# Kernel optimization log

Hardware: AMD Instinct MI355X
Metric: run time of the kernel (lower is better)

Reference implementation:

```python
import jax, jax.numpy as jnp
from jax import lax
import numpy as np

ALPHA = 0.5
MAX_ITERS = 40
TOL = 1e-6
BITS = 8


def fake_quant_sym(w, bits=BITS):
    # symmetric per-tensor fake quantisation
    qmax = float(2 ** (bits - 1) - 1)
    scale = jnp.max(jnp.abs(w)) / qmax
    return jnp.round(w / scale) * scale


def fb_solve(Wq, Uq, bq, x, alpha=ALPHA, max_iters=MAX_ITERS, tol=TOL):
    # forward-backward splitting fixed-point solve: z = relu((1-a)z + a(Wz + Ux^T + b))
    n = Wq.shape[0]
    B = x.shape[0]
    Ux = Uq @ x.T + bq[:, None]  # (n, B), constant across iterations

    def cond(carry):
        z, res, it = carry
        return jnp.logical_and(it < max_iters, res >= tol)

    def body(carry):
        z, _, it = carry
        u = (1.0 - alpha) * z + alpha * (Wq @ z + Ux)
        z_next = jax.nn.relu(u)  # relu_prox
        res = jnp.linalg.norm(z_next - z) / (jnp.linalg.norm(z) + 1e-12)
        return z_next, res, it + 1

    z0 = jnp.zeros((n, B), dtype=x.dtype)
    z, _, _ = lax.while_loop(cond, body, (z0, jnp.array(jnp.inf, dtype=x.dtype), 0))
    u_star = (1.0 - alpha) * z + alpha * (Wq @ z + Ux)
    mask = (u_star > 0).astype(x.dtype)  # relu Jacobian mask D*
    return z, mask


def setup_inputs() -> dict:
    key = jax.random.key(0)
    k0, k1, k2, k3, k4 = jax.random.split(key, 5)
    n, d, B, C = 512, 784, 128, 10
    # scale W so ||W||_2 < 1 (monotone operator condition m > 0)
    W = 0.3 * jax.random.normal(k0, (n, n), dtype=jnp.float32) / jnp.sqrt(n)
    U = jax.random.normal(k1, (n, d), dtype=jnp.float32) / jnp.sqrt(d)
    b = 0.01 * jax.random.normal(k2, (n,), dtype=jnp.float32)
    x = jax.random.normal(k3, (B, d), dtype=jnp.float32)
    Wc = jax.random.normal(k4, (C, n), dtype=jnp.float32) / jnp.sqrt(n)
    bc = jnp.zeros((C,), dtype=jnp.float32)
    return {"W": W, "U": U, "b": b, "x": x, "Wc": Wc, "bc": bc}


def reference(W, U, b, x, Wc, bc):
    # post-training fake quantisation of W, U, b (done once at init in torch)
    Wq = fake_quant_sym(W)
    Uq = fake_quant_sym(U)
    bq = fake_quant_sym(b)
    z_star, _ = fb_solve(Wq, Uq, bq, x)  # (n, B)
    logits = z_star.T @ Wc.T + bc  # classifier on z*^T
    return logits
```

## Files before the change

kernel.cpp:

```cpp
#include <hip/hip_runtime.h>
#include <hip/hip_bf16.h>


#define N_DIM 512
#define D_DIM 784
#define B_DIM 128
#define C_DIM 10
#define QMAX 127.0f
#define N_ITERS 40
#define HILO_START 28
#define ZPITCH 528
#define MT 2
#define XPITCH 800
#define QUPITCH 808

typedef int    i32x4  __attribute__((ext_vector_type(4)));
typedef float  f32x4  __attribute__((ext_vector_type(4)));
typedef __bf16 bf16x8 __attribute__((ext_vector_type(8)));
typedef short  s16x2  __attribute__((ext_vector_type(2)));

#define WSF_PW  0
#define WSF_PU  64
#define WSF_SB  128
#define WSF_CNT 160
#define WSF_BQ  192
#define WSF_XH  704
#define WSF_XL  (WSF_XH + 51200)
#define WSF_QP8 (WSF_XL + 51200)
#define WSF_UXT (WSF_QP8 + 65536)

#define N_PRODUCERS 96

__device__ __forceinline__ float pscale64(const float* __restrict__ p) {
    float m = 0.0f;
#pragma unroll 16
    for (int i = 0; i < 64; ++i) m = fmaxf(m, p[i]);
    return m * (1.0f / QMAX);
}

__device__ __forceinline__ void pack_hl(const int vq[4], unsigned int& h, unsigned int& l) {
    int pk01, pk23;
#if __has_builtin(__builtin_amdgcn_cvt_pk_i16)
    union { s16x2 v; int i; } u0, u1;
    u0.v = __builtin_amdgcn_cvt_pk_i16(vq[0], vq[1]);
    u1.v = __builtin_amdgcn_cvt_pk_i16(vq[2], vq[3]);
    pk01 = u0.i; pk23 = u1.i;
#else
    asm("v_cvt_pk_i16_i32 %0, %1, %2" : "=v"(pk01) : "v"(vq[0]), "v"(vq[1]));
    asm("v_cvt_pk_i16_i32 %0, %1, %2" : "=v"(pk23) : "v"(vq[2]), "v"(vq[3]));
#endif
    h = __builtin_amdgcn_perm((unsigned int)pk23, (unsigned int)pk01, 0x07050301u);
    l = __builtin_amdgcn_perm((unsigned int)pk23, (unsigned int)pk01, 0x06040200u) ^ 0x80808080u;
}

__global__ __launch_bounds__(256) void scales_kernel(const float* __restrict__ W,
                                                     const float* __restrict__ U,
                                                     const float* __restrict__ b,
                                                     const float* __restrict__ x,
                                                     float* __restrict__ ws) {
    __shared__ float ls[4];
    __shared__ float sbS;
    const int t = threadIdx.x, wave = t >> 6, lane = t & 63;
    const int bid = blockIdx.x;
    if (bid < 128) {
        const float4* src; int n4, rb;
        if (bid < 64) { src = (const float4*)W; n4 = N_DIM * N_DIM / 4; rb = bid; }
        else          { src = (const float4*)U; n4 = N_DIM * D_DIM / 4; rb = bid - 64; }
        float mv = 0.0f;
        for (int i = rb * 256 + t; i < n4; i += 64 * 256) {
            float4 v = src[i];
            mv = fmaxf(mv, fmaxf(fmaxf(fabsf(v.x), fabsf(v.y)), fmaxf(fabsf(v.z), fabsf(v.w))));
        }
#pragma unroll
        for (int s = 1; s < 64; s <<= 1) mv = fmaxf(mv, __shfl_xor(mv, s));
        if (lane == 0) ls[wave] = mv;
        __syncthreads();
        if (t == 0) ws[bid] = fmaxf(fmaxf(ls[0], ls[1]), fmaxf(ls[2], ls[3]));
    } else if (bid == 128) {
        if (t == 0) ((int*)ws)[WSF_CNT] = 0;
        float4 v = {0.0f, 0.0f, 0.0f, 0.0f};
        if (t < N_DIM / 4) v = ((const float4*)b)[t];
        float mv = fmaxf(fmaxf(fabsf(v.x), fabsf(v.y)), fmaxf(fabsf(v.z), fabsf(v.w)));
#pragma unroll
        for (int s = 1; s < 64; s <<= 1) mv = fmaxf(mv, __shfl_xor(mv, s));
        if (lane == 0) ls[wave] = mv;
        __syncthreads();
        if (t == 0) {
            float m = fmaxf(fmaxf(ls[0], ls[1]), fmaxf(ls[2], ls[3]));
            float sb = m * (1.0f / QMAX);
            ws[WSF_SB] = sb;
            sbS = sb;
        }
        __syncthreads();
        if (t < N_DIM / 4) {
            const float sb = sbS;
            float4 o;
            o.x = rintf(v.x / sb) * sb;
            o.y = rintf(v.y / sb) * sb;
            o.z = rintf(v.z / sb) * sb;
            o.w = rintf(v.w / sb) * sb;
            ((float4*)(ws + WSF_BQ))[t] = o;
        }
    } else {
        __bf16* xh = (__bf16*)(ws + WSF_XH);
        __bf16* xl = (__bf16*)(ws + WSF_XL);
        const int xb = bid - 129;
        for (int i = xb * 256 + t; i < 128 * 196; i += 64 * 256) {
            int r = i / 196, kf = i - r * 196;
            float4 v = *(const float4*)&x[r * D_DIM + (kf << 2)];
            union { __bf16 e[4]; ushort4 u; } hh, ll;
            __bf16 h0 = (__bf16)v.x, h1 = (__bf16)v.y, h2 = (__bf16)v.z, h3 = (__bf16)v.w;
            hh.e[0] = h0; hh.e[1] = h1; hh.e[2] = h2; hh.e[3] = h3;
            ll.e[0] = (__bf16)(v.x - (float)h0);
            ll.e[1] = (__bf16)(v.y - (float)h1);
            ll.e[2] = (__bf16)(v.z - (float)h2);
            ll.e[3] = (__bf16)(v.w - (float)h3);
            *(ushort4*)&xh[r * XPITCH + (kf << 2)] = hh.u;
            *(ushort4*)&xl[r * XPITCH + (kf << 2)] = ll.u;
        }
        if (xb == 0) {
            int r = t >> 1, c = D_DIM + (t & 1) * 8;
            ushort4 z = {0, 0, 0, 0};
            *(ushort4*)&xh[r * XPITCH + c] = z; *(ushort4*)&xh[r * XPITCH + c + 4] = z;
            *(ushort4*)&xl[r * XPITCH + c] = z; *(ushort4*)&xl[r * XPITCH + c + 4] = z;
        }
    }
}

__global__ __launch_bounds__(1024, 1) void fused_kernel(const float* __restrict__ W,
                                                        const float* __restrict__ U,
                                                        float* __restrict__ ws,
                                                        const float* __restrict__ Wc,
                                                        const float* __restrict__ bc,
                                                        float* __restrict__ out) {
    __shared__ __align__(16) char LDS[44032];
    const int t = threadIdx.x;
    const int wave = t >> 6, lane = t & 63;
    const int bid = blockIdx.x;
    signed char* Qp8 = (signed char*)(ws + WSF_QP8);
    int* cnt = (int*)ws + WSF_CNT;

    if (bid < 64) {
        const float s = pscale64(ws + WSF_PW);
        const float inv = 1.0f / s;
        int idx = bid * 1024 + t;
        float4 w = ((const float4*)W)[idx];
        int k = (idx << 2) & (N_DIM - 1);
        int r = (idx << 2) >> 9;
        char4 c;
        c.x = (signed char)(int)rintf(w.x * inv);
        c.y = (signed char)(int)rintf(w.y * inv);
        c.z = (signed char)(int)rintf(w.z * inv);
        c.w = (signed char)(int)rintf(w.w * inv);
        int kc = k >> 6, q = (k >> 4) & 3, jj = k & 15;
        *(char4*)&Qp8[((kc << 9) + r) * 64 + q * 16 + jj] = c;
        __syncthreads();
        if (t == 0) __hip_atomic_fetch_add(cnt, 1, __ATOMIC_RELEASE, __HIP_MEMORY_SCOPE_AGENT);
        return;
    }
    if (bid < 96) {
        __bf16 (*quS)[QUPITCH] = (__bf16 (*)[QUPITCH])LDS;
        const float sU = pscale64(ws + WSF_PU);
        const float invU = 1.0f / sU;
        const int i0 = (bid - 64) * 16;
        for (int i = t; i < 16 * 196; i += 1024) {
            int r = i / 196, kf = i - r * 196;
            float4 v = *(const float4*)&U[(i0 + r) * D_DIM + (kf << 2)];
            union { __bf16 e[4]; ushort4 u; } q;
            q.e[0] = (__bf16)rintf(v.x * invU);
            q.e[1] = (__bf16)rintf(v.y * invU);
            q.e[2] = (__bf16)rintf(v.z * invU);
            q.e[3] = (__bf16)rintf(v.w * invU);
            *(ushort4*)&quS[r][kf << 2] = q.u;
        }
        if (t < 256) { int r = t >> 4, k = D_DIM + (t & 15); quS[r][k] = (__bf16)0.0f; }
        __syncthreads();
        if (wave < 8) {
            const int m = lane & 15, quad = lane >> 4;
            const __bf16* xh = (const __bf16*)(ws + WSF_XH);
            const __bf16* xl = (const __bf16*)(ws + WSF_XL);
            const float* bq = ws + WSF_BQ;
            float* UxT = ws + WSF_UXT;
            const int row0 = i0 + (quad << 2);
            const f32x4 bqv = *(const f32x4*)&bq[row0];
            const int cg = wave;
            const __bf16* xhr = &xh[(cg * 16 + m) * XPITCH];
            const __bf16* xlr = &xl[(cg * 16 + m) * XPITCH];
            f32x4 acc = {};
#pragma unroll 5
            for (int kc = 0; kc < 25; ++kc) {
                bf16x8 au = *(const bf16x8*)&quS[m][kc * 32 + (quad << 3)];
                bf16x8 bh = *(const bf16x8*)&xhr[kc * 32 + (quad << 3)];
                bf16x8 bl = *(const bf16x8*)&xlr[kc * 32 + (quad << 3)];
                acc = __builtin_amdgcn_mfma_f32_16x16x32_bf16(au, bh, acc, 0, 0, 0);
                acc = __builtin_amdgcn_mfma_f32_16x16x32_bf16(au, bl, acc, 0, 0, 0);
            }
            f32x4 o;
#pragma unroll
            for (int r = 0; r < 4; ++r) o[r] = sU * acc[r] + bqv[r];
            *(f32x4*)&UxT[(cg * 16 + m) * N_DIM + row0] = o;
        }
        __syncthreads();
        if (t == 0) __hip_atomic_fetch_add(cnt, 1, __ATOMIC_RELEASE, __HIP_MEMORY_SCOPE_AGENT);
        return;
    }

    if (t == 0) {
        while (__hip_atomic_load(cnt, __ATOMIC_RELAXED, __HIP_MEMORY_SCOPE_AGENT) < N_PRODUCERS)
            __builtin_amdgcn_s_sleep(8);
    }
    __syncthreads();
    (void)__hip_atomic_load(cnt, __ATOMIC_ACQUIRE, __HIP_MEMORY_SCOPE_AGENT);

    signed char (*zh)[16][ZPITCH] = (signed char (*)[16][ZPITCH])(LDS);
    signed char (*zl)[16][ZPITCH] = (signed char (*)[16][ZPITCH])(LDS + 16896);
    float (*red)[16][C_DIM]       = (float (*)[16][C_DIM])(LDS + 33792);
    const float* UxT = ws + WSF_UXT;
    const int m = lane & 15;
    const int quad = lane >> 4;
    const int c0 = (bid - 96) * 16;
    const float sW = pscale64(ws + WSF_PW);
    const float c1 = sW * (1.0f / 2048.0f);
    const float hc_hi = c1 * 128.0f;
    const float g_hi = sW * 128.0f;
    const float g_lo = sW * 0.5f;
    const int rowbase = wave * 32;

    i32x4 A[MT][8];
#pragma unroll
    for (int ti = 0; ti < MT; ++ti)
#pragma unroll
        for (int kc = 0; kc < 8; ++kc)
            A[ti][kc] = *(const i32x4*)&Qp8[((kc << 9) + rowbase + ti * 16 + m) * 64 + (quad << 4)];

    const i32x4 onesb = {0x01010101, 0x01010101, 0x01010101, 0x01010101};
    i32x4 rs[MT];
#pragma unroll
    for (int ti = 0; ti < MT; ++ti) {
        i32x4 a = {};
#pragma unroll
        for (int kc = 0; kc < 8; ++kc)
            a = __builtin_amdgcn_mfma_i32_16x16x64_i8(A[ti][kc], onesb, a, 0, 0, 0);
        rs[ti] = a;
    }

    float Z[MT][4];
    float UX2[MT][4];
#pragma unroll
    for (int ti = 0; ti < MT; ++ti) {
        const int row0 = rowbase + ti * 16 + (quad << 2);
        const f32x4 v4 = *(const f32x4*)&UxT[(c0 + m) * N_DIM + row0];
        int vq[4];
#pragma unroll
        for (int r = 0; r < 4; ++r) {
            const float v = v4[r];
            const float uxh = 0.5f * (v + hc_hi * (float)rs[ti][r]);
            UX2[ti][r] = uxh * 2048.0f;
            const float z1 = fmaxf(0.5f * v, 0.0f);
            const float Z1 = z1 * 2048.0f;
            Z[ti][r] = Z1;
            vq[r] = (int)rintf(Z1);
        }
        unsigned int h, l;
        pack_hl(vq, h, l);
        *(unsigned int*)&zh[0][m][row0] = h;
        *(unsigned int*)&zl[0][m][row0] = l;
    }

#pragma unroll
    for (int ti = 0; ti < MT; ++ti)
#pragma unroll
        for (int kc = 0; kc < 8; ++kc)
            asm volatile("" : "+v"(A[ti][kc]));
    __syncthreads();

    int cur = 0;
    for (int it = 1; it < N_ITERS; ++it) {
        const bool lo = (it >= HILO_START);
        const bool wlo = (it >= HILO_START - 1);
        i32x4 acch[MT] = {};
        i32x4 accl[MT] = {};
        if (lo) {
#pragma unroll
            for (int kc = 0; kc < 8; ++kc) {
                i32x4 bh = *(const i32x4*)&zh[cur][m][(kc << 6) + (quad << 4)];
                i32x4 bl = *(const i32x4*)&zl[cur][m][(kc << 6) + (quad << 4)];
#pragma unroll
                for (int ti = 0; ti < MT; ++ti) {
                    acch[ti] = __builtin_amdgcn_mfma_i32_16x16x64_i8(A[ti][kc], bh, acch[ti], 0, 0, 0);
                    accl[ti] = __builtin_amdgcn_mfma_i32_16x16x64_i8(A[ti][kc], bl, accl[ti], 0, 0, 0);
                }
            }
        } else {
#pragma unroll
            for (int kc = 0; kc < 8; ++kc) {
                i32x4 bh = *(const i32x4*)&zh[cur][m][(kc << 6) + (quad << 4)];
#pragma unroll
                for (int ti = 0; ti < MT; ++ti)
                    acch[ti] = __builtin_amdgcn_mfma_i32_16x16x64_i8(A[ti][kc], bh, acch[ti], 0, 0, 0);
            }
        }
        const int nxt = cur ^ 1;
#pragma unroll
        for (int ti = 0; ti < MT; ++ti) {
            const int row0 = rowbase + ti * 16 + (quad << 2);
            int vq[4];
#pragma unroll
            for (int r = 0; r < 4; ++r) {
                float base = fmaf(0.5f, Z[ti][r], UX2[ti][r]);
                float u = lo ? fmaf(g_hi, (float)acch[ti][r], fmaf(g_lo, (float)accl[ti][r], base))
                             : fmaf(g_hi, (float)acch[ti][r], base);
                float Zn = fmaxf(u, 0.0f);
                Z[ti][r] = Zn;
                vq[r] = (int)rintf(Zn);
            }
            unsigned int h, l;
            pack_hl(vq, h, l);
            *(unsigned int*)&zh[nxt][m][row0] = h;
            if (wlo) *(unsigned int*)&zl[nxt][m][row0] = l;
        }
        __syncthreads();
        cur = nxt;
    }

    {
        float p[C_DIM];
#pragma unroll
        for (int cl = 0; cl < C_DIM; ++cl) p[cl] = 0.0f;
#pragma unroll
        for (int ti = 0; ti < MT; ++ti) {
            const int row0 = rowbase + ti * 16 + (quad << 2);
#pragma unroll
            for (int r = 0; r < 4; ++r) {
                float zv = Z[ti][r] * (1.0f / 2048.0f);
#pragma unroll
                for (int cl = 0; cl < C_DIM; ++cl)
                    p[cl] += zv * Wc[cl * N_DIM + row0 + r];
            }
        }
#pragma unroll
        for (int cl = 0; cl < C_DIM; ++cl) {
            p[cl] += __shfl_xor(p[cl], 16);
            p[cl] += __shfl_xor(p[cl], 32);
        }
        if (lane < 16) {
#pragma unroll
            for (int cl = 0; cl < C_DIM; ++cl) red[wave][lane][cl] = p[cl];
        }
        __syncthreads();
        for (int s = 8; s > 0; s >>= 1) {
            if (wave < s && lane < 16) {
#pragma unroll
                for (int cl = 0; cl < C_DIM; ++cl)
                    red[wave][lane][cl] += red[wave + s][lane][cl];
            }
            __syncthreads();
        }
        if (t < 16 * C_DIM) {
            int col = t & 15;
            int cl  = t >> 4;
            out[(c0 + col) * C_DIM + cl] = red[0][col][cl] + bc[cl];
        }
    }
}

extern "C" void kernel_launch(void* const* d_in, const int* in_sizes, int n_in,
                              void* d_out, int out_size, void* d_ws, size_t ws_size,
                              hipStream_t stream) {
    const float* W  = (const float*)d_in[0];
    const float* U  = (const float*)d_in[1];
    const float* b  = (const float*)d_in[2];
    const float* x  = (const float*)d_in[3];
    const float* Wc = (const float*)d_in[4];
    const float* bc = (const float*)d_in[5];
    float* out = (float*)d_out;
    float* ws = (float*)d_ws;

    scales_kernel<<<193, 256, 0, stream>>>(W, U, b, x, ws);
    fused_kernel<<<104, 1024, 0, stream>>>(W, U, ws, Wc, bc, out);
}
```

Baseline: 141.4 us.

## Split producer counters, widen U blocks, stagger K order, stage Wc in LDS

Producer completion now uses separate counters for the W-quantisation blocks and the Ux blocks. Consumers wait on the W counter before loading A fragments and computing row sums, and on the U counter only afterwards, so that setup overlaps the Ux computation. Ux producer blocks go from 32 to 16, each handling 32 rows with all 16 waves busy, and the grid shrinks from 104 to 88 blocks. Each wave starts its K loop at a different chunk to spread LDS bank access, and Wc is copied into LDS for the classifier epilogue, which adds LDS use.

```diff
diff --git a/kernel.cpp b/kernel.cpp
--- a/kernel.cpp
+++ b/kernel.cpp
@@ -19,17 +19,19 @@
 typedef __bf16 bf16x8 __attribute__((ext_vector_type(8)));
 typedef short  s16x2  __attribute__((ext_vector_type(2)));
 
-#define WSF_PW  0
-#define WSF_PU  64
-#define WSF_SB  128
-#define WSF_CNT 160
-#define WSF_BQ  192
-#define WSF_XH  704
-#define WSF_XL  (WSF_XH + 51200)
-#define WSF_QP8 (WSF_XL + 51200)
-#define WSF_UXT (WSF_QP8 + 65536)
-
-#define N_PRODUCERS 96
+#define WSF_PW   0
+#define WSF_PU   64
+#define WSF_SB   128
+#define WSF_CNTW 160
+#define WSF_CNTU 224
+#define WSF_BQ   288
+#define WSF_XH   800
+#define WSF_XL   (WSF_XH + 51200)
+#define WSF_QP8  (WSF_XL + 51200)
+#define WSF_UXT  (WSF_QP8 + 65536)
+
+#define N_PW 64
+#define N_PU 16
 
 __device__ __forceinline__ float pscale64(const float* __restrict__ p) {
     float m = 0.0f;
@@ -77,7 +79,7 @@
         __syncthreads();
         if (t == 0) ws[bid] = fmaxf(fmaxf(ls[0], ls[1]), fmaxf(ls[2], ls[3]));
     } else if (bid == 128) {
-        if (t == 0) ((int*)ws)[WSF_CNT] = 0;
+        if (t == 0) { ((int*)ws)[WSF_CNTW] = 0; ((int*)ws)[WSF_CNTU] = 0; }
         float4 v = {0.0f, 0.0f, 0.0f, 0.0f};
         if (t < N_DIM / 4) v = ((const float4*)b)[t];
         float mv = fmaxf(fmaxf(fabsf(v.x), fabsf(v.y)), fmaxf(fabsf(v.z), fabsf(v.w)));
@@ -133,12 +135,13 @@
                                                         const float* __restrict__ Wc,
                                                         const float* __restrict__ bc,
                                                         float* __restrict__ out) {
-    __shared__ __align__(16) char LDS[44032];
+    __shared__ __align__(16) char LDS[54272];
     const int t = threadIdx.x;
     const int wave = t >> 6, lane = t & 63;
     const int bid = blockIdx.x;
     signed char* Qp8 = (signed char*)(ws + WSF_QP8);
-    int* cnt = (int*)ws + WSF_CNT;
+    int* cntW = (int*)ws + WSF_CNTW;
+    int* cntU = (int*)ws + WSF_CNTU;
 
     if (bid < 64) {
         const float s = pscale64(ws + WSF_PW);
@@ -155,15 +158,15 @@
         int kc = k >> 6, q = (k >> 4) & 3, jj = k & 15;
         *(char4*)&Qp8[((kc << 9) + r) * 64 + q * 16 + jj] = c;
         __syncthreads();
-        if (t == 0) __hip_atomic_fetch_add(cnt, 1, __ATOMIC_RELEASE, __HIP_MEMORY_SCOPE_AGENT);
+        if (t == 0) __hip_atomic_fetch_add(cntW, 1, __ATOMIC_RELEASE, __HIP_MEMORY_SCOPE_AGENT);
         return;
     }
-    if (bid < 96) {
+    if (bid < 80) {
         __bf16 (*quS)[QUPITCH] = (__bf16 (*)[QUPITCH])LDS;
         const float sU = pscale64(ws + WSF_PU);
         const float invU = 1.0f / sU;
-        const int i0 = (bid - 64) * 16;
-        for (int i = t; i < 16 * 196; i += 1024) {
+        const int i0 = (bid - 64) * 32;
+        for (int i = t; i < 32 * 196; i += 1024) {
             int r = i / 196, kf = i - r * 196;
             float4 v = *(const float4*)&U[(i0 + r) * D_DIM + (kf << 2)];
             union { __bf16 e[4]; ushort4 u; } q;
@@ -173,23 +176,24 @@
             q.e[3] = (__bf16)rintf(v.w * invU);
             *(ushort4*)&quS[r][kf << 2] = q.u;
         }
-        if (t < 256) { int r = t >> 4, k = D_DIM + (t & 15); quS[r][k] = (__bf16)0.0f; }
-        __syncthreads();
-        if (wave < 8) {
+        if (t < 512) { int r = t >> 4, k = D_DIM + (t & 15); quS[r][k] = (__bf16)0.0f; }
+        __syncthreads();
+        {
             const int m = lane & 15, quad = lane >> 4;
+            const int rh = wave >> 3;
+            const int cg = wave & 7;
             const __bf16* xh = (const __bf16*)(ws + WSF_XH);
             const __bf16* xl = (const __bf16*)(ws + WSF_XL);
             const float* bq = ws + WSF_BQ;
             float* UxT = ws + WSF_UXT;
-            const int row0 = i0 + (quad << 2);
+            const int row0 = i0 + rh * 16 + (quad << 2);
             const f32x4 bqv = *(const f32x4*)&bq[row0];
-            const int cg = wave;
             const __bf16* xhr = &xh[(cg * 16 + m) * XPITCH];
             const __bf16* xlr = &xl[(cg * 16 + m) * XPITCH];
             f32x4 acc = {};
 #pragma unroll 5
             for (int kc = 0; kc < 25; ++kc) {
-                bf16x8 au = *(const bf16x8*)&quS[m][kc * 32 + (quad << 3)];
+                bf16x8 au = *(const bf16x8*)&quS[rh * 16 + m][kc * 32 + (quad << 3)];
                 bf16x8 bh = *(const bf16x8*)&xhr[kc * 32 + (quad << 3)];
                 bf16x8 bl = *(const bf16x8*)&xlr[kc * 32 + (quad << 3)];
                 acc = __builtin_amdgcn_mfma_f32_16x16x32_bf16(au, bh, acc, 0, 0, 0);
@@ -201,24 +205,18 @@
             *(f32x4*)&UxT[(cg * 16 + m) * N_DIM + row0] = o;
         }
         __syncthreads();
-        if (t == 0) __hip_atomic_fetch_add(cnt, 1, __ATOMIC_RELEASE, __HIP_MEMORY_SCOPE_AGENT);
+        if (t == 0) __hip_atomic_fetch_add(cntU, 1, __ATOMIC_RELEASE, __HIP_MEMORY_SCOPE_AGENT);
         return;
     }
-
-    if (t == 0) {
-        while (__hip_atomic_load(cnt, __ATOMIC_RELAXED, __HIP_MEMORY_SCOPE_AGENT) < N_PRODUCERS)
-            __builtin_amdgcn_s_sleep(8);
-    }
-    __syncthreads();
-    (void)__hip_atomic_load(cnt, __ATOMIC_ACQUIRE, __HIP_MEMORY_SCOPE_AGENT);
 
     signed char (*zh)[16][ZPITCH] = (signed char (*)[16][ZPITCH])(LDS);
     signed char (*zl)[16][ZPITCH] = (signed char (*)[16][ZPITCH])(LDS + 16896);
-    float (*red)[16][C_DIM]       = (float (*)[16][C_DIM])(LDS + 33792);
+    float* WcS                    = (float*)(LDS + 33792);
+    float (*red)[16][C_DIM]       = (float (*)[16][C_DIM])(LDS);
     const float* UxT = ws + WSF_UXT;
     const int m = lane & 15;
     const int quad = lane >> 4;
-    const int c0 = (bid - 96) * 16;
+    const int c0 = (bid - 80) * 16;
     const float sW = pscale64(ws + WSF_PW);
     const float c1 = sW * (1.0f / 2048.0f);
     const float hc_hi = c1 * 128.0f;
@@ -226,12 +224,24 @@
     const float g_lo = sW * 0.5f;
     const int rowbase = wave * 32;
 
+    if (t == 0) {
+        while (__hip_atomic_load(cntW, __ATOMIC_RELAXED, __HIP_MEMORY_SCOPE_AGENT) < N_PW)
+            __builtin_amdgcn_s_sleep(8);
+    }
+    __syncthreads();
+    (void)__hip_atomic_load(cntW, __ATOMIC_ACQUIRE, __HIP_MEMORY_SCOPE_AGENT);
+
+    const int kst = wave & 7;
+    int kidx[8];
+#pragma unroll
+    for (int j = 0; j < 8; ++j) kidx[j] = (j + kst) & 7;
+
     i32x4 A[MT][8];
 #pragma unroll
     for (int ti = 0; ti < MT; ++ti)
 #pragma unroll
-        for (int kc = 0; kc < 8; ++kc)
-            A[ti][kc] = *(const i32x4*)&Qp8[((kc << 9) + rowbase + ti * 16 + m) * 64 + (quad << 4)];
+        for (int j = 0; j < 8; ++j)
+            A[ti][j] = *(const i32x4*)&Qp8[((kidx[j] << 9) + rowbase + ti * 16 + m) * 64 + (quad << 4)];
 
     const i32x4 onesb = {0x01010101, 0x01010101, 0x01010101, 0x01010101};
     i32x4 rs[MT];
@@ -239,10 +249,19 @@
     for (int ti = 0; ti < MT; ++ti) {
         i32x4 a = {};
 #pragma unroll
-        for (int kc = 0; kc < 8; ++kc)
-            a = __builtin_amdgcn_mfma_i32_16x16x64_i8(A[ti][kc], onesb, a, 0, 0, 0);
+        for (int j = 0; j < 8; ++j)
+            a = __builtin_amdgcn_mfma_i32_16x16x64_i8(A[ti][j], onesb, a, 0, 0, 0);
         rs[ti] = a;
     }
+
+    for (int i = t; i < C_DIM * N_DIM; i += 1024) WcS[i] = Wc[i];
+
+    if (t == 0) {
+        while (__hip_atomic_load(cntU, __ATOMIC_RELAXED, __HIP_MEMORY_SCOPE_AGENT) < N_PU)
+            __builtin_amdgcn_s_sleep(8);
+    }
+    __syncthreads();
+    (void)__hip_atomic_load(cntU, __ATOMIC_ACQUIRE, __HIP_MEMORY_SCOPE_AGENT);
 
     float Z[MT][4];
     float UX2[MT][4];
@@ -270,8 +289,8 @@
 #pragma unroll
     for (int ti = 0; ti < MT; ++ti)
 #pragma unroll
-        for (int kc = 0; kc < 8; ++kc)
-            asm volatile("" : "+v"(A[ti][kc]));
+        for (int j = 0; j < 8; ++j)
+            asm volatile("" : "+v"(A[ti][j]));
     __syncthreads();
 
     int cur = 0;
@@ -282,22 +301,24 @@
         i32x4 accl[MT] = {};
         if (lo) {
 #pragma unroll
-            for (int kc = 0; kc < 8; ++kc) {
-                i32x4 bh = *(const i32x4*)&zh[cur][m][(kc << 6) + (quad << 4)];
-                i32x4 bl = *(const i32x4*)&zl[cur][m][(kc << 6) + (quad << 4)];
+            for (int j = 0; j < 8; ++j) {
+                const int ka = (kidx[j] << 6) + (quad << 4);
+                i32x4 bh = *(const i32x4*)&zh[cur][m][ka];
+                i32x4 bl = *(const i32x4*)&zl[cur][m][ka];
 #pragma unroll
                 for (int ti = 0; ti < MT; ++ti) {
-                    acch[ti] = __builtin_amdgcn_mfma_i32_16x16x64_i8(A[ti][kc], bh, acch[ti], 0, 0, 0);
-                    accl[ti] = __builtin_amdgcn_mfma_i32_16x16x64_i8(A[ti][kc], bl, accl[ti], 0, 0, 0);
+                    acch[ti] = __builtin_amdgcn_mfma_i32_16x16x64_i8(A[ti][j], bh, acch[ti], 0, 0, 0);
+                    accl[ti] = __builtin_amdgcn_mfma_i32_16x16x64_i8(A[ti][j], bl, accl[ti], 0, 0, 0);
                 }
             }
         } else {
 #pragma unroll
-            for (int kc = 0; kc < 8; ++kc) {
-                i32x4 bh = *(const i32x4*)&zh[cur][m][(kc << 6) + (quad << 4)];
+            for (int j = 0; j < 8; ++j) {
+                const int ka = (kidx[j] << 6) + (quad << 4);
+                i32x4 bh = *(const i32x4*)&zh[cur][m][ka];
 #pragma unroll
                 for (int ti = 0; ti < MT; ++ti)
-                    acch[ti] = __builtin_amdgcn_mfma_i32_16x16x64_i8(A[ti][kc], bh, acch[ti], 0, 0, 0);
+                    acch[ti] = __builtin_amdgcn_mfma_i32_16x16x64_i8(A[ti][j], bh, acch[ti], 0, 0, 0);
             }
         }
         const int nxt = cur ^ 1;
@@ -335,7 +356,7 @@
                 float zv = Z[ti][r] * (1.0f / 2048.0f);
 #pragma unroll
                 for (int cl = 0; cl < C_DIM; ++cl)
-                    p[cl] += zv * Wc[cl * N_DIM + row0 + r];
+                    p[cl] += zv * WcS[cl * N_DIM + row0 + r];
             }
         }
 #pragma unroll
@@ -377,5 +398,5 @@
     float* ws = (float*)d_ws;
 
     scales_kernel<<<193, 256, 0, stream>>>(W, U, b, x, ws);
-    fused_kernel<<<104, 1024, 0, stream>>>(W, U, ws, Wc, bc, out);
+    fused_kernel<<<88, 1024, 0, stream>>>(W, U, ws, Wc, bc, out);
 }
```

After: 141.5 us. About the same (+0.1%).
